# Performance work log

Hardware: AMD Instinct MI355X
Metric: run time of the kernel (lower is better)

The kernel has to match this reference:

```python
import jax, jax.numpy as jnp
import numpy as np

N_NODES = 100000
N_EDGES = 1200000
N_GRAPHS = 1024
IN_FEATS = 64
HID = 64
BN_EPS = 1e-5


def setup_inputs() -> dict:
    key = jax.random.key(0)
    ks = jax.random.split(key, 20)
    feats = jax.random.normal(ks[0], (N_NODES, IN_FEATS), jnp.float32)
    src = jax.random.randint(ks[1], (N_EDGES,), 0, N_NODES, jnp.int32)
    dst = jax.random.randint(ks[2], (N_EDGES,), 0, N_NODES, jnp.int32)
    graph_ids = jnp.sort(jax.random.randint(ks[3], (N_NODES,), 0, N_GRAPHS, jnp.int32))

    def lin(k, fi, fo):
        s = 1.0 / np.sqrt(fi)
        kw, kb = jax.random.split(k)
        return (jax.random.uniform(kw, (fi, fo), jnp.float32, -s, s),
                jax.random.uniform(kb, (fo,), jnp.float32, -s, s))

    W_self, _ = lin(ks[4], IN_FEATS, HID)
    W_neigh, b_neigh = lin(ks[5], IN_FEATS, HID)
    W1, b1 = lin(ks[6], HID, 128)
    W2, b2 = lin(ks[7], 128, 64)
    W3, b3 = lin(ks[8], 64, 1)

    def bn(k, d):
        k1, k2, k3, k4 = jax.random.split(k, 4)
        return (jax.random.normal(k1, (d,), jnp.float32) * 0.1 + 1.0,
                jax.random.normal(k2, (d,), jnp.float32) * 0.1,
                jax.random.normal(k3, (d,), jnp.float32) * 0.1,
                jax.random.uniform(k4, (d,), jnp.float32, 0.5, 1.5))

    g1, be1, rm1, rv1 = bn(ks[9], 128)
    g2, be2, rm2, rv2 = bn(ks[10], 64)

    return dict(feats=feats, src=src, dst=dst, graph_ids=graph_ids,
                W_self=W_self, W_neigh=W_neigh, b_neigh=b_neigh,
                W1=W1, b1=b1, g1=g1, be1=be1, rm1=rm1, rv1=rv1,
                W2=W2, b2=b2, g2=g2, be2=be2, rm2=rm2, rv2=rv2,
                W3=W3, b3=b3)


def reference(feats, src, dst, graph_ids, W_self, W_neigh, b_neigh,
              W1, b1, g1, be1, rm1, rv1, W2, b2, g2, be2, rm2, rv2, W3, b3):
    # --- SAGEConv (mean aggregator): h = W_self@h_self + W_neigh@mean_neigh + b
    deg = jax.ops.segment_sum(jnp.ones((src.shape[0],), feats.dtype), dst,
                              num_segments=N_NODES)                      # [N]
    agg = jax.ops.segment_sum(feats[src], dst, num_segments=N_NODES)     # [N, F]
    mean_neigh = agg / jnp.maximum(deg, 1.0)[:, None]
    h = feats @ W_self + mean_neigh @ W_neigh + b_neigh
    h = jax.nn.relu(h)                                                   # activation

    # --- per-graph max readout (dgl.max_nodes)
    hg = jax.ops.segment_max(h, graph_ids, num_segments=N_GRAPHS)        # [G, HID]

    # --- MLP head with eval-mode BatchNorm1d
    def bn(x, g, b, rm, rv):
        return (x - rm) * jax.lax.rsqrt(rv + BN_EPS) * g + b

    x = bn(jax.nn.relu(hg @ W1 + b1), g1, be1, rm1, rv1)
    x = bn(jax.nn.relu(x @ W2 + b2), g2, be2, rm2, rv2)
    return x @ W3 + b3                                                   # [G, n_task]
```

## Files before the change

kernel.cpp:

```cpp
#include <hip/hip_runtime.h>
#include <hip/hip_fp16.h>

#define N_NODES  100000
#define N_EDGES  1200000
#define N_GRAPHS 1024
#define F        64
#define BN_EPS   1e-5f
#define NBUCK    ((N_NODES + 255) / 256)
#define NBLK     512
#define CHUNK    ((N_EDGES + NBLK - 1) / NBLK)
#define MT       128
#define GEMM_BLOCKS ((N_NODES + MT - 1) / MT)
#define CE       3584
#define LDA      72

typedef _Float16 f16x8 __attribute__((ext_vector_type(8)));
typedef float f32x4 __attribute__((ext_vector_type(4)));

__global__ __launch_bounds__(256) void prep(
    const float* __restrict__ feats, const float* __restrict__ Wself,
    const float* __restrict__ Wneigh, __half* __restrict__ Uh,
    __half* __restrict__ Zh, const int* __restrict__ dst,
    int* __restrict__ Ct, int* __restrict__ hgbits) {
  __shared__ __align__(16) char smraw[2 * 128 * LDA * 2];
  int t = threadIdx.x;

  if (blockIdx.x >= GEMM_BLOCKS) {
    int* lh = (int*)smraw;
    int b = blockIdx.x - GEMM_BLOCKS;
    int zidx = b * 256 + t;
    if (zidx < N_GRAPHS * F) hgbits[zidx] = 0;
    for (int i = t; i < NBUCK; i += 256) lh[i] = 0;
    __syncthreads();
    int e0 = b * CHUNK, e1 = e0 + CHUNK;
    if (e1 > N_EDGES) e1 = N_EDGES;
    for (int e = e0 + t; e < e1; e += 256) atomicAdd(&lh[dst[e] >> 8], 1);
    __syncthreads();
    for (int i = t; i < NBUCK; i += 256) Ct[(size_t)b * NBUCK + i] = lh[i];
    return;
  }

  __half* As = (__half*)smraw;
  __half* Bs = As + 128 * LDA;
  int mbase = blockIdx.x * MT;

#pragma unroll
  for (int s = 0; s < 8; s++) {
    int idx = s * 256 + t;
    int row = idx >> 4, c4 = idx & 15;
    int gm = mbase + row;
    float4 v = (gm < N_NODES) ? *(const float4*)(feats + (size_t)gm * F + c4 * 4)
                              : make_float4(0.f, 0.f, 0.f, 0.f);
    union { __half h[4]; uint2 u; } pk;
    pk.h[0] = __float2half_rn(v.x); pk.h[1] = __float2half_rn(v.y);
    pk.h[2] = __float2half_rn(v.z); pk.h[3] = __float2half_rn(v.w);
    *(uint2*)(As + row * LDA + c4 * 4) = pk.u;
  }

#pragma unroll
  for (int s = 0; s < 2; s++) {
    int unit = s * 256 + t;
    int kq = unit >> 5, c4 = unit & 31;
    const float* Wp = (c4 < 16) ? (Wself + c4 * 4) : (Wneigh + (c4 - 16) * 4);
    float4 w0 = *(const float4*)(Wp + (kq * 4 + 0) * 64);
    float4 w1 = *(const float4*)(Wp + (kq * 4 + 1) * 64);
    float4 w2 = *(const float4*)(Wp + (kq * 4 + 2) * 64);
    float4 w3 = *(const float4*)(Wp + (kq * 4 + 3) * 64);
    float a[4][4] = {{w0.x, w0.y, w0.z, w0.w}, {w1.x, w1.y, w1.z, w1.w},
                     {w2.x, w2.y, w2.z, w2.w}, {w3.x, w3.y, w3.z, w3.w}};
#pragma unroll
    for (int c = 0; c < 4; c++) {
      union { __half h[4]; uint2 u; } pk;
      pk.h[0] = __float2half_rn(a[0][c]); pk.h[1] = __float2half_rn(a[1][c]);
      pk.h[2] = __float2half_rn(a[2][c]); pk.h[3] = __float2half_rn(a[3][c]);
      *(uint2*)(Bs + (c4 * 4 + c) * LDA + kq * 4) = pk.u;
    }
  }
  __syncthreads();

  int wave = t >> 6, lane = t & 63;
  int lr = lane & 15, kg = lane >> 4;
  int r0 = wave * 32;

  f32x4 acc[2][8];
#pragma unroll
  for (int i = 0; i < 2; i++)
#pragma unroll
    for (int j = 0; j < 8; j++) acc[i][j] = (f32x4){0.f, 0.f, 0.f, 0.f};

#pragma unroll
  for (int h = 0; h < 2; h++) {
    f16x8 a0 = *(const f16x8*)(As + (r0 + lr) * LDA + h * 32 + kg * 8);
    f16x8 a1 = *(const f16x8*)(As + (r0 + 16 + lr) * LDA + h * 32 + kg * 8);
#pragma unroll
    for (int j = 0; j < 8; j++) {
      f16x8 wv = *(const f16x8*)(Bs + (j * 16 + lr) * LDA + h * 32 + kg * 8);
      acc[0][j] = __builtin_amdgcn_mfma_f32_16x16x32_f16(wv, a0, acc[0][j], 0, 0, 0);
      acc[1][j] = __builtin_amdgcn_mfma_f32_16x16x32_f16(wv, a1, acc[1][j], 0, 0, 0);
    }
  }

#pragma unroll
  for (int i = 0; i < 2; i++) {
    int node = mbase + r0 + i * 16 + lr;
    if (node < N_NODES) {
#pragma unroll
      for (int j = 0; j < 8; j++) {
        int f = j * 16 + kg * 4;
        union { __half h[4]; uint2 u; } pk;
        pk.h[0] = __float2half_rn(acc[i][j][0]);
        pk.h[1] = __float2half_rn(acc[i][j][1]);
        pk.h[2] = __float2half_rn(acc[i][j][2]);
        pk.h[3] = __float2half_rn(acc[i][j][3]);
        __half* outp = (f < 64) ? (Uh + (size_t)node * F + f)
                                : (Zh + (size_t)node * F + (f - 64));
        *(uint2*)outp = pk.u;
      }
    }
  }
}

__global__ __launch_bounds__(NBLK) void cscan(int* __restrict__ Ct,
                                              int* __restrict__ bcnt) {
  __shared__ int s[NBLK];
  int i = blockIdx.x, t = threadIdx.x;
  int v = Ct[(size_t)t * NBUCK + i];
  s[t] = v;
  __syncthreads();
  for (int off = 1; off < NBLK; off <<= 1) {
    int u = (t >= off) ? s[t - off] : 0;
    __syncthreads();
    s[t] += u;
    __syncthreads();
  }
  Ct[(size_t)t * NBUCK + i] = s[t] - v;
  if (t == NBLK - 1) bcnt[i] = s[NBLK - 1];
}

__global__ __launch_bounds__(512) void bscan(const int* __restrict__ bcnt,
                                             int* __restrict__ bstart) {
  __shared__ int s[512];
  int t = threadIdx.x;
  int v = (t < NBUCK) ? bcnt[t] : 0;
  s[t] = v;
  __syncthreads();
  for (int off = 1; off < 512; off <<= 1) {
    int u = (t >= off) ? s[t - off] : 0;
    __syncthreads();
    s[t] += u;
    __syncthreads();
  }
  if (t < NBUCK) bstart[t] = s[t] - v;
  if (t == 0) bstart[NBUCK] = N_EDGES;
}

__global__ __launch_bounds__(256) void cscat(const int* __restrict__ src,
                                             const int* __restrict__ dst,
                                             const int* __restrict__ Ct,
                                             const int* __restrict__ bstart,
                                             int* __restrict__ pairs) {
  __shared__ int cur[NBUCK];
  int b = blockIdx.x, t = threadIdx.x;
  for (int i = t; i < NBUCK; i += 256)
    cur[i] = bstart[i] + Ct[(size_t)b * NBUCK + i];
  __syncthreads();
  int e0 = b * CHUNK, e1 = e0 + CHUNK;
  if (e1 > N_EDGES) e1 = N_EDGES;
  for (int e = e0 + t; e < e1; e += 256) {
    int d = dst[e];
    int pos = atomicAdd(&cur[d >> 8], 1);
    pairs[pos] = (int)((((unsigned)d & 255u) << 24) | (unsigned)src[e]);
  }
}

__global__ __launch_bounds__(1024) void gather_place(
    const __half* __restrict__ Uh, const __half* __restrict__ Zh,
    const int* __restrict__ pairs, const int* __restrict__ bstart,
    const float* __restrict__ bneigh, const int* __restrict__ gids,
    int* __restrict__ hgbits) {
  __shared__ int eidx_l[CE];
  __shared__ int rsl[256];
  __shared__ int lh[256];
  __shared__ int cur[256];
  int b = blockIdx.x, t = threadIdx.x;
  int nb0 = b << 8;
  int r0 = bstart[b], r1 = bstart[b + 1];
  int E = r1 - r0; if (E > CE) E = CE;

  if (t < 256) lh[t] = 0;
  __syncthreads();
  for (int e = t; e < E; e += 1024)
    atomicAdd(&lh[((unsigned)pairs[r0 + e]) >> 24], 1);
  __syncthreads();
  if (t < 256) cur[t] = lh[t];
  __syncthreads();
  for (int off = 1; off < 256; off <<= 1) {
    int u = (t < 256 && t >= off) ? cur[t - off] : 0;
    __syncthreads();
    if (t < 256) cur[t] += u;
    __syncthreads();
  }
  if (t < 256) { int ex = cur[t] - lh[t]; rsl[t] = ex; cur[t] = ex; }
  __syncthreads();
  for (int e = t; e < E; e += 1024) {
    unsigned p = (unsigned)pairs[r0 + e];
    int pos = atomicAdd(&cur[p >> 24], 1);
    eidx_l[pos] = (int)(p & 0xFFFFFFu);
  }
  __syncthreads();

  int wave = t >> 6, lane = t & 63;
  int fl = lane & 15, sub = lane >> 4;
  float4 b4 = *(const float4*)(bneigh + 4 * fl);
  int nl = wave * 16;
  int nend = nl + 16;
  if (nb0 + nl >= N_NODES) return;
  if (nb0 + nend > N_NODES) nend = N_NODES - nb0;

  int curg = gids[nb0 + nl];
  float4 gmax = {0.f, 0.f, 0.f, 0.f};

  for (; nl < nend; nl++) {
    int node = nb0 + nl;
    int rr  = rsl[nl];
    int deg = lh[nl];
    uint2 ur = *(const uint2*)(Uh + (size_t)node * F + 4 * fl);
    float sx = 0.f, sy = 0.f, sz = 0.f, sw = 0.f;
    for (int jj = 0; jj < deg; jj += 16) {
      int j0 = jj + sub;
      int s0 = (j0      < deg) ? eidx_l[rr + j0]      : 0;
      int s1 = (j0 + 4  < deg) ? eidx_l[rr + j0 + 4]  : 0;
      int s2 = (j0 + 8  < deg) ? eidx_l[rr + j0 + 8]  : 0;
      int s3 = (j0 + 12 < deg) ? eidx_l[rr + j0 + 12] : 0;
      uint2 z0 = *(const uint2*)(Zh + (size_t)s0 * F + 4 * fl);
      uint2 z1 = *(const uint2*)(Zh + (size_t)s1 * F + 4 * fl);
      uint2 z2 = *(const uint2*)(Zh + (size_t)s2 * F + 4 * fl);
      uint2 z3 = *(const uint2*)(Zh + (size_t)s3 * F + 4 * fl);
      if (j0 < deg) {
        float2 f0 = __half22float2(*(__half2*)&z0.x);
        float2 f1 = __half22float2(*(__half2*)&z0.y);
        sx += f0.x; sy += f0.y; sz += f1.x; sw += f1.y;
      }
      if (j0 + 4 < deg) {
        float2 f0 = __half22float2(*(__half2*)&z1.x);
        float2 f1 = __half22float2(*(__half2*)&z1.y);
        sx += f0.x; sy += f0.y; sz += f1.x; sw += f1.y;
      }
      if (j0 + 8 < deg) {
        float2 f0 = __half22float2(*(__half2*)&z2.x);
        float2 f1 = __half22float2(*(__half2*)&z2.y);
        sx += f0.x; sy += f0.y; sz += f1.x; sw += f1.y;
      }
      if (j0 + 12 < deg) {
        float2 f0 = __half22float2(*(__half2*)&z3.x);
        float2 f1 = __half22float2(*(__half2*)&z3.y);
        sx += f0.x; sy += f0.y; sz += f1.x; sw += f1.y;
      }
    }
    sx += __shfl_xor(sx, 16); sy += __shfl_xor(sy, 16);
    sz += __shfl_xor(sz, 16); sw += __shfl_xor(sw, 16);
    sx += __shfl_xor(sx, 32); sy += __shfl_xor(sy, 32);
    sz += __shfl_xor(sz, 32); sw += __shfl_xor(sw, 32);
    float inv = 1.0f / fmaxf((float)deg, 1.0f);

    int g = gids[node];
    if (g != curg) {
      if (sub == 0) {
        int* hp = hgbits + (size_t)curg * F + 4 * fl;
        atomicMax(hp + 0, __float_as_int(gmax.x));
        atomicMax(hp + 1, __float_as_int(gmax.y));
        atomicMax(hp + 2, __float_as_int(gmax.z));
        atomicMax(hp + 3, __float_as_int(gmax.w));
      }
      curg = g; gmax = make_float4(0.f, 0.f, 0.f, 0.f);
    }

    float2 uf0 = __half22float2(*(__half2*)&ur.x);
    float2 uf1 = __half22float2(*(__half2*)&ur.y);
    gmax.x = fmaxf(gmax.x, fmaxf(uf0.x + sx * inv + b4.x, 0.f));
    gmax.y = fmaxf(gmax.y, fmaxf(uf0.y + sy * inv + b4.y, 0.f));
    gmax.z = fmaxf(gmax.z, fmaxf(uf1.x + sz * inv + b4.z, 0.f));
    gmax.w = fmaxf(gmax.w, fmaxf(uf1.y + sw * inv + b4.w, 0.f));
  }
  if (sub == 0) {
    int* hp = hgbits + (size_t)curg * F + 4 * fl;
    atomicMax(hp + 0, __float_as_int(gmax.x));
    atomicMax(hp + 1, __float_as_int(gmax.y));
    atomicMax(hp + 2, __float_as_int(gmax.z));
    atomicMax(hp + 3, __float_as_int(gmax.w));
  }
}

#define GPB 8
__global__ __launch_bounds__(128) void mlp(
    const float* __restrict__ hg,
    const float* __restrict__ W1, const float* __restrict__ b1,
    const float* __restrict__ g1, const float* __restrict__ be1,
    const float* __restrict__ rm1, const float* __restrict__ rv1,
    const float* __restrict__ W2, const float* __restrict__ b2,
    const float* __restrict__ g2, const float* __restrict__ be2,
    const float* __restrict__ rm2, const float* __restrict__ rv2,
    const float* __restrict__ W3, const float* __restrict__ b3,
    float* __restrict__ out) {
  __shared__ float W1s[64 * 128];
  __shared__ float W2s[128 * 64];
  __shared__ float W3s[64];
  __shared__ float sc1[128], sh1[128], b1s[128];
  __shared__ float sc2[64],  sh2[64],  b2s[64];
  __shared__ float s0[64], s1[128], s2[64];
  int t = threadIdx.x;

  for (int i = t; i < 64 * 128; i += 128) W1s[i] = W1[i];
  for (int i = t; i < 128 * 64; i += 128) W2s[i] = W2[i];
  if (t < 64) W3s[t] = W3[t];
  {
    float iv = rsqrtf(rv1[t] + BN_EPS);
    float sc = g1[t] * iv;
    sc1[t] = sc; sh1[t] = be1[t] - rm1[t] * sc; b1s[t] = b1[t];
  }
  if (t < 64) {
    float iv = rsqrtf(rv2[t] + BN_EPS);
    float sc = g2[t] * iv;
    sc2[t] = sc; sh2[t] = be2[t] - rm2[t] * sc; b2s[t] = b2[t];
  }
  __syncthreads();

  for (int gg = 0; gg < GPB; gg++) {
    int g = blockIdx.x * GPB + gg;
    if (t < 64) s0[t] = hg[(size_t)g * F + t];
    __syncthreads();
    {
      float acc = b1s[t];
      for (int i = 0; i < 64; i++) acc += s0[i] * W1s[i * 128 + t];
      acc = fmaxf(acc, 0.0f);
      s1[t] = acc * sc1[t] + sh1[t];
    }
    __syncthreads();
    if (t < 64) {
      float acc = b2s[t];
      for (int i = 0; i < 128; i++) acc += s1[i] * W2s[i * 64 + t];
      acc = fmaxf(acc, 0.0f);
      s2[t] = acc * sc2[t] + sh2[t];
    }
    __syncthreads();
    if (t < 64) {
      float p = s2[t] * W3s[t];
      for (int off = 32; off > 0; off >>= 1) p += __shfl_down(p, off);
      if (t == 0) out[g] = p + b3[0];
    }
    __syncthreads();
  }
}

extern "C" void kernel_launch(void* const* d_in, const int* in_sizes, int n_in,
                              void* d_out, int out_size, void* d_ws, size_t ws_size,
                              hipStream_t stream) {
  const float* feats  = (const float*)d_in[0];
  const int*   src    = (const int*)d_in[1];
  const int*   dst    = (const int*)d_in[2];
  const int*   gids   = (const int*)d_in[3];
  const float* Wself  = (const float*)d_in[4];
  const float* Wneigh = (const float*)d_in[5];
  const float* bneigh = (const float*)d_in[6];
  const float* W1  = (const float*)d_in[7];
  const float* b1  = (const float*)d_in[8];
  const float* g1  = (const float*)d_in[9];
  const float* be1 = (const float*)d_in[10];
  const float* rm1 = (const float*)d_in[11];
  const float* rv1 = (const float*)d_in[12];
  const float* W2  = (const float*)d_in[13];
  const float* b2  = (const float*)d_in[14];
  const float* g2  = (const float*)d_in[15];
  const float* be2 = (const float*)d_in[16];
  const float* rm2 = (const float*)d_in[17];
  const float* rv2 = (const float*)d_in[18];
  const float* W3  = (const float*)d_in[19];
  const float* b3  = (const float*)d_in[20];

  __half* Uh   = (__half*)d_ws;
  __half* Zh   = Uh + (size_t)N_NODES * F;
  int* bstart  = (int*)(Zh + (size_t)N_NODES * F);
  int* bcnt    = bstart + (NBUCK + 1);
  int* hgbits  = bcnt + NBUCK;
  int* Ct      = hgbits + (size_t)N_GRAPHS * F;
  int* pairs   = Ct + (size_t)NBLK * NBUCK;

  prep<<<GEMM_BLOCKS + NBLK, 256, 0, stream>>>(feats, Wself, Wneigh, Uh, Zh,
                                               dst, Ct, hgbits);
  cscan<<<NBUCK, NBLK, 0, stream>>>(Ct, bcnt);
  bscan<<<1, 512, 0, stream>>>(bcnt, bstart);
  cscat<<<NBLK, 256, 0, stream>>>(src, dst, Ct, bstart, pairs);
  gather_place<<<NBUCK, 1024, 0, stream>>>(Uh, Zh, pairs, bstart, bneigh,
                                           gids, hgbits);
  mlp<<<N_GRAPHS / GPB, 128, 0, stream>>>((const float*)hgbits,
                                          W1, b1, g1, be1, rm1, rv1,
                                          W2, b2, g2, be2, rm2, rv2, W3, b3,
                                          (float*)d_out);
}
```

Baseline: 212.8 us.

## Replace per-block count scans with global atomic bucket counts and fused scatter

Bucket counts are now accumulated with global atomics during prep, and a single scat kernel scans the global counts, reserves per-block slots through atomicAdd on a cursor array, and scatters the edges. This removes the cscan and bscan kernels and the per-block count matrix, cutting two launches and their memory traffic. Slot reservation makes the edge order inside each bucket nondeterministic, which could change float summation order downstream. A memset is added, and the MLP graphs-per-block drops from 8 to 2 to launch more blocks.

```diff
diff --git a/kernel.cpp b/kernel.cpp
--- a/kernel.cpp
+++ b/kernel.cpp
@@ -21,7 +21,7 @@
     const float* __restrict__ feats, const float* __restrict__ Wself,
     const float* __restrict__ Wneigh, __half* __restrict__ Uh,
     __half* __restrict__ Zh, const int* __restrict__ dst,
-    int* __restrict__ Ct, int* __restrict__ hgbits) {
+    int* __restrict__ bcnt, int* __restrict__ hgbits) {
   __shared__ __align__(16) char smraw[2 * 128 * LDA * 2];
   int t = threadIdx.x;
 
@@ -36,7 +36,10 @@
     if (e1 > N_EDGES) e1 = N_EDGES;
     for (int e = e0 + t; e < e1; e += 256) atomicAdd(&lh[dst[e] >> 8], 1);
     __syncthreads();
-    for (int i = t; i < NBUCK; i += 256) Ct[(size_t)b * NBUCK + i] = lh[i];
+    for (int i = t; i < NBUCK; i += 256) {
+      int c = lh[i];
+      if (c) atomicAdd(&bcnt[i], c);
+    }
     return;
   }
 
@@ -120,54 +123,42 @@
   }
 }
 
-__global__ __launch_bounds__(NBLK) void cscan(int* __restrict__ Ct,
-                                              int* __restrict__ bcnt) {
-  __shared__ int s[NBLK];
-  int i = blockIdx.x, t = threadIdx.x;
-  int v = Ct[(size_t)t * NBUCK + i];
-  s[t] = v;
-  __syncthreads();
-  for (int off = 1; off < NBLK; off <<= 1) {
-    int u = (t >= off) ? s[t - off] : 0;
-    __syncthreads();
-    s[t] += u;
-    __syncthreads();
-  }
-  Ct[(size_t)t * NBUCK + i] = s[t] - v;
-  if (t == NBLK - 1) bcnt[i] = s[NBLK - 1];
-}
-
-__global__ __launch_bounds__(512) void bscan(const int* __restrict__ bcnt,
-                                             int* __restrict__ bstart) {
-  __shared__ int s[512];
-  int t = threadIdx.x;
-  int v = (t < NBUCK) ? bcnt[t] : 0;
-  s[t] = v;
-  __syncthreads();
-  for (int off = 1; off < 512; off <<= 1) {
-    int u = (t >= off) ? s[t - off] : 0;
-    __syncthreads();
-    s[t] += u;
-    __syncthreads();
-  }
-  if (t < NBUCK) bstart[t] = s[t] - v;
-  if (t == 0) bstart[NBUCK] = N_EDGES;
-}
-
-__global__ __launch_bounds__(256) void cscat(const int* __restrict__ src,
-                                             const int* __restrict__ dst,
-                                             const int* __restrict__ Ct,
-                                             const int* __restrict__ bstart,
-                                             int* __restrict__ pairs) {
+__global__ __launch_bounds__(512) void scat(
+    const int* __restrict__ src, const int* __restrict__ dst,
+    const int* __restrict__ bcnt, int* __restrict__ gcur,
+    int* __restrict__ pairs, int* __restrict__ bstart) {
+  __shared__ int sc[512];
+  __shared__ int lh[NBUCK];
   __shared__ int cur[NBUCK];
+  __shared__ int dcache[CHUNK];
   int b = blockIdx.x, t = threadIdx.x;
-  for (int i = t; i < NBUCK; i += 256)
-    cur[i] = bstart[i] + Ct[(size_t)b * NBUCK + i];
+  if (t < NBUCK) lh[t] = 0;
   __syncthreads();
   int e0 = b * CHUNK, e1 = e0 + CHUNK;
   if (e1 > N_EDGES) e1 = N_EDGES;
-  for (int e = e0 + t; e < e1; e += 256) {
+  for (int e = e0 + t; e < e1; e += 512) {
     int d = dst[e];
+    dcache[e - e0] = d;
+    atomicAdd(&lh[d >> 8], 1);
+  }
+  int v = (t < NBUCK) ? bcnt[t] : 0;
+  sc[t] = v;
+  __syncthreads();
+  for (int off = 1; off < 512; off <<= 1) {
+    int u = (t >= off) ? sc[t - off] : 0;
+    __syncthreads();
+    sc[t] += u;
+    __syncthreads();
+  }
+  if (t < NBUCK) {
+    int base = sc[t] - v;
+    cur[t] = base + atomicAdd(&gcur[t], lh[t]);
+    if (b == 0) bstart[t] = base;
+  }
+  if (b == 0 && t == 0) bstart[NBUCK] = N_EDGES;
+  __syncthreads();
+  for (int e = e0 + t; e < e1; e += 512) {
+    int d = dcache[e - e0];
     int pos = atomicAdd(&cur[d >> 8], 1);
     pairs[pos] = (int)((((unsigned)d & 255u) << 24) | (unsigned)src[e]);
   }
@@ -291,7 +282,7 @@
   }
 }
 
-#define GPB 8
+#define GPB 2
 __global__ __launch_bounds__(128) void mlp(
     const float* __restrict__ hg,
     const float* __restrict__ W1, const float* __restrict__ b1,
@@ -381,15 +372,15 @@
   __half* Zh   = Uh + (size_t)N_NODES * F;
   int* bstart  = (int*)(Zh + (size_t)N_NODES * F);
   int* bcnt    = bstart + (NBUCK + 1);
-  int* hgbits  = bcnt + NBUCK;
-  int* Ct      = hgbits + (size_t)N_GRAPHS * F;
-  int* pairs   = Ct + (size_t)NBLK * NBUCK;
+  int* gcur    = bcnt + NBUCK;
+  int* hgbits  = gcur + NBUCK;
+  int* pairs   = hgbits + (size_t)N_GRAPHS * F;
+
+  hipMemsetAsync(bcnt, 0, 2 * NBUCK * sizeof(int), stream);
 
   prep<<<GEMM_BLOCKS + NBLK, 256, 0, stream>>>(feats, Wself, Wneigh, Uh, Zh,
-                                               dst, Ct, hgbits);
-  cscan<<<NBUCK, NBLK, 0, stream>>>(Ct, bcnt);
-  bscan<<<1, 512, 0, stream>>>(bcnt, bstart);
-  cscat<<<NBLK, 256, 0, stream>>>(src, dst, Ct, bstart, pairs);
+                                               dst, bcnt, hgbits);
+  scat<<<NBLK, 512, 0, stream>>>(src, dst, bcnt, gcur, pairs, bstart);
   gather_place<<<NBUCK, 1024, 0, stream>>>(Uh, Zh, pairs, bstart, bneigh,
                                            gids, hgbits);
   mlp<<<N_GRAPHS / GPB, 128, 0, stream>>>((const float*)hgbits,
```

New measurement: 209.0 us. About the same (-1.8%).
